# Kernel tuning notes

Measured on AMD Instinct MI355X. Metric: run time of the kernel, lower is better.

## Reference

```python
import jax, jax.numpy as jnp
import numpy as np

B, S, D = 4, 2048, 256
H = 8
HD = D // H
FF = 1024
LEN_M1 = 513


def _layer_norm(x, gamma, beta, eps=1e-5):
    m = jnp.mean(x, axis=-1, keepdims=True)
    v = jnp.var(x, axis=-1, keepdims=True)
    return (x - m) * jax.lax.rsqrt(v + eps) * gamma + beta


def setup_inputs() -> dict:
    key = jax.random.key(0)
    ks = jax.random.split(key, 16)
    s = 0.02  # init scale for weights
    return {
        "src": jax.random.normal(ks[0], (B, S, D), dtype=jnp.float32),
        "Wq": jax.random.normal(ks[1], (D, D), dtype=jnp.float32) * s,
        "bq": jnp.zeros((D,), dtype=jnp.float32),
        "Wk": jax.random.normal(ks[2], (D, D), dtype=jnp.float32) * s,
        "bk": jnp.zeros((D,), dtype=jnp.float32),
        "Wv": jax.random.normal(ks[3], (D, D), dtype=jnp.float32) * s,
        "bv": jnp.zeros((D,), dtype=jnp.float32),
        "Wo": jax.random.normal(ks[4], (D, D), dtype=jnp.float32) * s,
        "bo": jnp.zeros((D,), dtype=jnp.float32),
        "W1": jax.random.normal(ks[5], (FF, D), dtype=jnp.float32) * s,
        "b1": jnp.zeros((FF,), dtype=jnp.float32),
        "W2": jax.random.normal(ks[6], (D, FF), dtype=jnp.float32) * s,
        "b2": jnp.zeros((D,), dtype=jnp.float32),
        "g1": jnp.ones((D,), dtype=jnp.float32),
        "be1": jnp.zeros((D,), dtype=jnp.float32),
        "g2": jnp.ones((D,), dtype=jnp.float32),
        "be2": jnp.zeros((D,), dtype=jnp.float32),
        "len_m1": LEN_M1,
    }


def reference(src, Wq, bq, Wk, bk, Wv, bv, Wo, bo, W1, b1, W2, b2, g1, be1, g2, be2, len_m1):
    Bb, Ss, Dd = src.shape
    hd = Dd // H
    # projections (torch Linear: x @ W.T + b), split heads -> [B,H,S,hd]
    q = (src @ Wq.T + bq).reshape(Bb, Ss, H, hd).transpose(0, 2, 1, 3)
    k = (src @ Wk.T + bk).reshape(Bb, Ss, H, hd).transpose(0, 2, 1, 3)
    v = (src @ Wv.T + bv).reshape(Bb, Ss, H, hd).transpose(0, 2, 1, 3)
    scores = jnp.einsum("bhqd,bhkd->bhqk", q, k) / np.sqrt(hd).astype(np.float32)
    # causal mask + global prefix block: masked where j > i OR (i < len_m1 and j >= len_m1)
    i = jnp.arange(Ss)[:, None]
    j = jnp.arange(Ss)[None, :]
    mask = (j > i) | ((i < len_m1) & (j >= len_m1))
    scores = jnp.where(mask, -jnp.inf, scores)
    attn = jax.nn.softmax(scores, axis=-1)
    ao = jnp.einsum("bhqk,bhkd->bhqd", attn, v).transpose(0, 2, 1, 3).reshape(Bb, Ss, Dd)
    src2 = _layer_norm(src + (ao @ Wo.T + bo), g1, be1)
    ff = jax.nn.gelu(src2 @ W1.T + b1, approximate=False) @ W2.T + b2
    return _layer_norm(src2 + ff, g2, be2)
```

## Files before the change

### kernel.cpp

```cpp
#include <hip/hip_runtime.h>
#include <math.h>

#define NB 4
#define NS 2048
#define ND 256
#define NH 8
#define NHD 32
#define NFF 1024
#define NM (NB*NS)
#define KPAD 40
#define VSP 72
#define VTP 72
#define AS 264
#define QSCALE 0.2550181657f

typedef __attribute__((ext_vector_type(4))) short short4v;
typedef __attribute__((ext_vector_type(8))) short short8v;
typedef __attribute__((ext_vector_type(4))) float f32x4;
typedef unsigned short us;

__device__ __forceinline__ us f2bf(float f){
  union { float f; unsigned u; } c; c.f = f;
  unsigned u = c.u + 0x7fffu + ((c.u >> 16) & 1u);
  return (us)(u >> 16);
}

__device__ __forceinline__ float wsum(float v){
  #pragma unroll
  for(int o=32;o>0;o>>=1) v += __shfl_xor(v,o);
  return v;
}

__global__ __launch_bounds__(256) void prep_kernel(
    const float* __restrict__ src,
    const float* __restrict__ Wq, const float* __restrict__ Wk, const float* __restrict__ Wv,
    const float* __restrict__ Wo, const float* __restrict__ W1, const float* __restrict__ W2,
    const float* __restrict__ bq,
    us* __restrict__ X, us* __restrict__ Wqkvb, us* __restrict__ Wob,
    us* __restrict__ W1b, us* __restrict__ W2b, float* __restrict__ bqs){
  unsigned bid = blockIdx.x;
  if (bid == 1408){ bqs[threadIdx.x] = bq[threadIdx.x]*QSCALE; return; }
  unsigned u = bid*256u + threadIdx.x;
  const float* sp; us* dp; float sc = 1.f;
  if (u < 262144u){ sp = src + (size_t)u*8; dp = X + (size_t)u*8; }
  else {
    unsigned v = u - 262144u;
    if      (v <  8192u){ sp = Wq + (size_t)v*8;            dp = Wqkvb + (size_t)v*8;            sc = QSCALE; }
    else if (v < 16384u){ sp = Wk + (size_t)(v- 8192u)*8;   dp = Wqkvb + 65536 + (size_t)(v- 8192u)*8; }
    else if (v < 24576u){ sp = Wv + (size_t)(v-16384u)*8;   dp = Wqkvb + 131072 + (size_t)(v-16384u)*8; }
    else if (v < 32768u){ sp = Wo + (size_t)(v-24576u)*8;   dp = Wob + (size_t)(v-24576u)*8; }
    else if (v < 65536u){ sp = W1 + (size_t)(v-32768u)*8;   dp = W1b + (size_t)(v-32768u)*8; }
    else               { sp = W2 + (size_t)(v-65536u)*8;    dp = W2b + (size_t)(v-65536u)*8; }
  }
  float4 a = *(const float4*)sp, b = *(const float4*)(sp+4);
  short8v o;
  o[0]=(short)f2bf(a.x*sc); o[1]=(short)f2bf(a.y*sc); o[2]=(short)f2bf(a.z*sc); o[3]=(short)f2bf(a.w*sc);
  o[4]=(short)f2bf(b.x*sc); o[5]=(short)f2bf(b.y*sc); o[6]=(short)f2bf(b.z*sc); o[7]=(short)f2bf(b.w*sc);
  *(short8v*)dp = o;
}

template<int KTOT, int EPI>
__global__ __launch_bounds__(256) void gemm_kernel(
    const us* __restrict__ A, const us* __restrict__ W,
    const float* __restrict__ bias0, const float* __restrict__ bias1, const float* __restrict__ bias2,
    const float* __restrict__ resid,
    us* __restrict__ outb, us* __restrict__ outv, float* __restrict__ outf){
  __shared__ us Asl[64*AS];
  const int t = threadIdx.x, l = t&63, wv = t>>6;
  const int lx = l&15, lw = l>>4;
  const int m0 = blockIdx.y*64;
  const int n0 = blockIdx.x*128 + wv*32;

  f32x4 acc[4][2];
  #pragma unroll
  for(int mb=0;mb<4;mb++)
    #pragma unroll
    for(int nb=0;nb<2;nb++) acc[mb][nb] = (f32x4){0.f,0.f,0.f,0.f};

  for (int kc = 0; kc < KTOT; kc += 256){
    __syncthreads();
    #pragma unroll
    for (int it=0; it<8; it++){
      int idx = it*256 + t;
      int r = idx>>5, c = idx&31;
      *(short8v*)&Asl[r*AS + c*8] = *(const short8v*)(A + (size_t)(m0+r)*KTOT + kc + c*8);
    }
    __syncthreads();
    short8v bf[2][8];
    #pragma unroll
    for (int nb=0; nb<2; nb++)
      #pragma unroll
      for (int ks=0; ks<8; ks++)
        bf[nb][ks] = *(const short8v*)(W + (size_t)(n0 + nb*16 + lx)*KTOT + kc + ks*32 + 8*lw);
    #pragma unroll
    for (int ks=0; ks<8; ks++){
      short8v af[4];
      #pragma unroll
      for (int mb=0; mb<4; mb++)
        af[mb] = *(const short8v*)&Asl[(mb*16+lx)*AS + ks*32 + 8*lw];
      #pragma unroll
      for (int mb=0; mb<4; mb++){
        acc[mb][0] = __builtin_amdgcn_mfma_f32_16x16x32_bf16(af[mb], bf[0][ks], acc[mb][0], 0,0,0);
        acc[mb][1] = __builtin_amdgcn_mfma_f32_16x16x32_bf16(af[mb], bf[1][ks], acc[mb][1], 0,0,0);
      }
    }
  }
  const int mr0 = m0 + 4*lw;
  #pragma unroll
  for (int nb=0; nb<2; nb++){
    int n = n0 + nb*16 + lx;
    if (EPI == 0){
      int seg = n >> 8, nn = n & 255;
      const float* bp = (seg==0) ? bias0 : (seg==1) ? bias1 : bias2;
      float bb = bp[nn];
      if (seg < 2){
        us* op = outb + (size_t)seg*((size_t)NM*ND) + nn;
        #pragma unroll
        for (int mb=0; mb<4; mb++)
          #pragma unroll
          for (int r=0; r<4; r++)
            op[(size_t)(mr0 + mb*16 + r)*ND] = f2bf(acc[mb][nb][r] + bb);
      } else {
        int hh = nn >> 5, dd = nn & 31;
        int bidx = mr0 >> 11;
        int s0 = mr0 & 2047;
        us* vp = outv + (((size_t)bidx*NH + hh)*NHD + dd)*NS;
        #pragma unroll
        for (int mb=0; mb<4; mb++){
          short4v v4;
          #pragma unroll
          for (int r=0; r<4; r++) v4[r] = (short)f2bf(acc[mb][nb][r] + bb);
          *(short4v*)(vp + s0 + mb*16) = v4;
        }
      }
    } else if (EPI == 1 || EPI == 3){
      float bb = bias0[n];
      #pragma unroll
      for (int mb=0; mb<4; mb++)
        #pragma unroll
        for (int r=0; r<4; r++){
          size_t off = (size_t)(mr0 + mb*16 + r)*ND + n;
          outf[off] = acc[mb][nb][r] + bb + resid[off];
        }
    } else {
      float bb = bias0[n];
      #pragma unroll
      for (int mb=0; mb<4; mb++)
        #pragma unroll
        for (int r=0; r<4; r++){
          float x = acc[mb][nb][r] + bb;
          float g = 0.5f*x*(1.f + erff(x*0.70710678118654752f));
          outb[(size_t)(mr0 + mb*16 + r)*NFF + n] = f2bf(g);
        }
    }
  }
}

__global__ __launch_bounds__(256) void ln_kernel(
    const float* __restrict__ Xin, const float* __restrict__ g, const float* __restrict__ be,
    us* __restrict__ outb, float* __restrict__ outf){
  const int t = threadIdx.x, lane = t&63, wv = t>>6;
  const int m0 = blockIdx.x*16;
  #pragma unroll
  for(int rr=0; rr<4; rr++){
    int r = m0 + wv*4 + rr;
    const float* xr = Xin + (size_t)r*ND;
    float x[4]; float s=0.f,q=0.f;
    #pragma unroll
    for(int k=0;k<4;k++){ x[k]=xr[lane+64*k]; s+=x[k]; q+=x[k]*x[k]; }
    s = wsum(s); q = wsum(q);
    float mean = s*(1.f/ND), var = q*(1.f/ND)-mean*mean;
    float rstd = rsqrtf(var+1e-5f);
    #pragma unroll
    for(int k=0;k<4;k++){
      int col = lane+64*k;
      float y = (x[k]-mean)*rstd*g[col] + be[col];
      if (outf) outf[(size_t)r*ND+col] = y;
      if (outb) outb[(size_t)r*ND+col] = f2bf(y);
    }
  }
}

template<bool MASK>
__device__ __forceinline__ void attn_tile(
    const us* __restrict__ Kl, const us* __restrict__ Vl,
    const short8v qf, const int lx, const int lw, const int jt, const int qg,
    f32x4& acc0, f32x4& acc1, float& lsum){
  f32x4 s4[4];
  #pragma unroll
  for (int kb=0; kb<4; kb++){
    short8v kf = *(const short8v*)(Kl + (kb*16 + lx)*KPAD + 8*lw);
    f32x4 z = {0.f,0.f,0.f,0.f};
    s4[kb] = __builtin_amdgcn_mfma_f32_16x16x32_bf16(kf, qf, z, 0,0,0);
  }
  float p[16];
  #pragma unroll
  for (int kb=0; kb<4; kb++)
    #pragma unroll
    for (int r=0; r<4; r++){
      float x = exp2f(s4[kb][r]);
      if (MASK) x = ((jt + 16*kb + 4*lw + r) > qg) ? 0.f : x;
      p[kb*4+r] = x;
    }
  {
    float a0=p[0]+p[1],   a1=p[2]+p[3],   a2=p[4]+p[5],   a3=p[6]+p[7];
    float a4=p[8]+p[9],   a5=p[10]+p[11], a6=p[12]+p[13], a7=p[14]+p[15];
    float b0=a0+a1, b1=a2+a3, b2=a4+a5, b3=a6+a7;
    lsum += (b0+b1) + (b2+b3);
  }
  #pragma unroll
  for (int c=0; c<2; c++){
    unsigned w0,w1,w2,w3;
    asm("v_cvt_pk_bf16_f32 %0, %1, %2" : "=v"(w0) : "v"(p[8*c+0]), "v"(p[8*c+1]));
    asm("v_cvt_pk_bf16_f32 %0, %1, %2" : "=v"(w1) : "v"(p[8*c+2]), "v"(p[8*c+3]));
    asm("v_cvt_pk_bf16_f32 %0, %1, %2" : "=v"(w2) : "v"(p[8*c+4]), "v"(p[8*c+5]));
    asm("v_cvt_pk_bf16_f32 %0, %1, %2" : "=v"(w3) : "v"(p[8*c+6]), "v"(p[8*c+7]));
    union { unsigned u[4]; short8v v; } pu;
    pu.u[0]=w0; pu.u[1]=w1; pu.u[2]=w2; pu.u[3]=w3;
    short8v pf = pu.v;
    short8v aL = *(const short8v*)(Vl + (size_t)( lx    )*VSP + 32*c + 8*lw);
    short8v aH = *(const short8v*)(Vl + (size_t)(16+lx  )*VSP + 32*c + 8*lw);
    acc0 = __builtin_amdgcn_mfma_f32_16x16x32_bf16(aL, pf, acc0, 0,0,0);
    acc1 = __builtin_amdgcn_mfma_f32_16x16x32_bf16(aH, pf, acc1, 0,0,0);
  }
}

__global__ __launch_bounds__(256) void attn_kernel(
    const us* __restrict__ Q, const us* __restrict__ K,
    const us* __restrict__ Vt, us* __restrict__ AO){
  __shared__ us Klds[2][64*KPAD];
  __shared__ us Vs[2][32*VSP];
  __shared__ us Ex[4][16*VTP];

  const int t = threadIdx.x, l = t & 63, wv = t >> 6;
  const int lx = l & 15, lw = l >> 4;
  const int bid = blockIdx.x;
  const int qtile = 31 - (bid >> 5);
  const int bh = bid & 31;
  const int b = bh >> 3, h = bh & 7;
  const int qbase = qtile*64 + wv*16;
  const int qg = qbase + lx;

  const us* Qg = Q + ((size_t)b*NS)*ND + h*NHD;
  const us* Kg = K + ((size_t)b*NS)*ND + h*NHD;
  const us* Vg = Vt + (size_t)bh*NHD*NS;

  short8v qf = *(const short8v*)(Qg + (size_t)(qbase + lx)*ND + 8*lw);

  f32x4 acc0 = {0.f,0.f,0.f,0.f}, acc1 = {0.f,0.f,0.f,0.f};
  float lsum = 0.f;

  const int kr = t >> 2, kp = t & 3;
  const int vd = t >> 3, vp = t & 7;
  const int vS0 = 32*(vp>>2) + 16*(vp&1) + 4*((vp>>1)&1);
  const int jmax = qtile*64;

  {
    short8v k0 = *(const short8v*)(Kg + (size_t)kr*ND + kp*8);
    short8v v0 = *(const short8v*)(Vg + (size_t)vd*NS + vp*8);
    *(short8v*)&Klds[0][kr*KPAD + kp*8] = k0;
    short4v lo = {v0[0],v0[1],v0[2],v0[3]}, hi = {v0[4],v0[5],v0[6],v0[7]};
    *(short4v*)&Vs[0][vd*VSP + vS0]     = lo;
    *(short4v*)&Vs[0][vd*VSP + vS0 + 8] = hi;
  }
  __syncthreads();

  int cur = 0;
  for (int jt = 0; jt < jmax; jt += 64){
    short8v kn = *(const short8v*)(Kg + (size_t)(jt + 64 + kr)*ND + kp*8);
    short8v vn = *(const short8v*)(Vg + (size_t)vd*NS + (jt + 64) + vp*8);
    attn_tile<false>(&Klds[cur][0], &Vs[cur][0], qf, lx, lw, jt, qg, acc0, acc1, lsum);
    *(short8v*)&Klds[cur^1][kr*KPAD + kp*8] = kn;
    short4v lo = {vn[0],vn[1],vn[2],vn[3]}, hi = {vn[4],vn[5],vn[6],vn[7]};
    *(short4v*)&Vs[cur^1][vd*VSP + vS0]     = lo;
    *(short4v*)&Vs[cur^1][vd*VSP + vS0 + 8] = hi;
    __syncthreads();
    cur ^= 1;
  }
  attn_tile<true>(&Klds[cur][0], &Vs[cur][0], qf, lx, lw, jmax, qg, acc0, acc1, lsum);

  float lt = lsum + __shfl_xor(lsum, 16);
  lt += __shfl_xor(lt, 32);
  float inv = 1.f / lt;
  float* ol = (float*)&Ex[wv][0];
  #pragma unroll
  for (int r=0;r<4;r++){
    ol[lx*36 +      4*lw + r] = acc0[r]*inv;
    ol[lx*36 + 16 + 4*lw + r] = acc1[r]*inv;
  }
  int rr = l >> 2, cc = l & 3;
  const float* op8 = &ol[rr*36 + cc*8];
  short8v o8;
  #pragma unroll
  for (int j=0;j<8;j++) o8[j] = (short)f2bf(op8[j]);
  *(short8v*)(AO + ((size_t)(b*NS + qbase + rr))*ND + h*NHD + cc*8) = o8;
}

extern "C" void kernel_launch(void* const* d_in, const int* in_sizes, int n_in,
                              void* d_out, int out_size, void* d_ws, size_t ws_size,
                              hipStream_t stream){
  const float* src = (const float*)d_in[0];
  const float* Wq  = (const float*)d_in[1];
  const float* bq  = (const float*)d_in[2];
  const float* Wk  = (const float*)d_in[3];
  const float* bk  = (const float*)d_in[4];
  const float* Wv  = (const float*)d_in[5];
  const float* bv  = (const float*)d_in[6];
  const float* Wo  = (const float*)d_in[7];
  const float* bo  = (const float*)d_in[8];
  const float* W1  = (const float*)d_in[9];
  const float* b1  = (const float*)d_in[10];
  const float* W2  = (const float*)d_in[11];
  const float* b2  = (const float*)d_in[12];
  const float* g1  = (const float*)d_in[13];
  const float* be1 = (const float*)d_in[14];
  const float* g2  = (const float*)d_in[15];
  const float* be2 = (const float*)d_in[16];

  const size_t MB = 1048576;
  unsigned char* w8 = (unsigned char*)d_ws;
  us* X     = (us*)(w8 + 0);
  us* Qb    = (us*)(w8 + 4*MB);
  us* Kb    = (us*)(w8 + 8*MB);
  us* Vtg   = (us*)(w8 + 12*MB);
  us* AO    = (us*)(w8 + 16*MB);
  us* S2b   = (us*)(w8 + 20*MB);
  us* FF    = (us*)(w8 + 24*MB);
  us* Wqkvb = (us*)(w8 + 40*MB);
  us* Wob   = (us*)(w8 + 40*MB + 384*1024);
  us* W1b   = (us*)(w8 + 40*MB + 512*1024);
  us* W2b   = (us*)(w8 + 40*MB + 1024*1024);
  float* bqs   = (float*)(w8 + 40*MB + 1536*1024);
  float* S2pre = (float*)(w8 + 42*MB);
  float* S2f   = (float*)(w8 + 50*MB);
  float* Ypre  = (float*)(w8 + 0);
  float* out = (float*)d_out;

  prep_kernel<<<1409, 256, 0, stream>>>(src, Wq,Wk,Wv,Wo,W1,W2, bq,
                                        X, Wqkvb, Wob, W1b, W2b, bqs);
  gemm_kernel<256,0><<<dim3(6,128), 256, 0, stream>>>(X, Wqkvb, bqs, bk, bv, nullptr, Qb, Vtg, nullptr);
  attn_kernel<<<1024, 256, 0, stream>>>(Qb, Kb, Vtg, AO);
  gemm_kernel<256,1><<<dim3(2,128), 256, 0, stream>>>(AO, Wob, bo, nullptr, nullptr, src, nullptr, nullptr, S2pre);
  ln_kernel<<<NM/16, 256, 0, stream>>>(S2pre, g1, be1, S2b, S2f);
  gemm_kernel<256,2><<<dim3(8,128), 256, 0, stream>>>(S2b, W1b, b1, nullptr, nullptr, nullptr, FF, nullptr, nullptr);
  gemm_kernel<1024,3><<<dim3(2,128), 256, 0, stream>>>(FF, W2b, b2, nullptr, nullptr, S2f, nullptr, nullptr, Ypre);
  ln_kernel<<<NM/16, 256, 0, stream>>>(Ypre, g2, be2, nullptr, out);
}
```

Measured before the change: 106.5 us.

## Pair query tiles per attention block and read FFN residual as bf16

The attention kernel now runs 512-thread blocks that each handle two adjacent 64-row query tiles of one head. The K/V tiles are staged once for both tiles, with half the threads loading K and half loading V, and each wave applies the causal mask on its own diagonal tile. This halves redundant K/V global loads and LDS staging, and the new block ordering pairs early and late tiles to balance causal work. Separately, the final FFN GEMM reads the residual from the bf16 LayerNorm output instead of a separate fp32 copy, which drops one fp32 write and read but adds bf16 rounding error to the residual.

```diff
diff --git a/kernel.cpp b/kernel.cpp
--- a/kernel.cpp
+++ b/kernel.cpp
@@ -23,6 +23,9 @@
   union { float f; unsigned u; } c; c.f = f;
   unsigned u = c.u + 0x7fffu + ((c.u >> 16) & 1u);
   return (us)(u >> 16);
+}
+__device__ __forceinline__ float bf2f(us u){
+  union { unsigned u; float f; } c; c.u = ((unsigned)u) << 16; return c.f;
 }
 
 __device__ __forceinline__ float wsum(float v){
@@ -63,7 +66,7 @@
 __global__ __launch_bounds__(256) void gemm_kernel(
     const us* __restrict__ A, const us* __restrict__ W,
     const float* __restrict__ bias0, const float* __restrict__ bias1, const float* __restrict__ bias2,
-    const float* __restrict__ resid,
+    const float* __restrict__ resid, const us* __restrict__ residb,
     us* __restrict__ outb, us* __restrict__ outv, float* __restrict__ outf){
   __shared__ us Asl[64*AS];
   const int t = threadIdx.x, l = t&63, wv = t>>6;
@@ -133,7 +136,7 @@
           *(short4v*)(vp + s0 + mb*16) = v4;
         }
       }
-    } else if (EPI == 1 || EPI == 3){
+    } else if (EPI == 1){
       float bb = bias0[n];
       #pragma unroll
       for (int mb=0; mb<4; mb++)
@@ -141,6 +144,15 @@
         for (int r=0; r<4; r++){
           size_t off = (size_t)(mr0 + mb*16 + r)*ND + n;
           outf[off] = acc[mb][nb][r] + bb + resid[off];
+        }
+    } else if (EPI == 3){
+      float bb = bias0[n];
+      #pragma unroll
+      for (int mb=0; mb<4; mb++)
+        #pragma unroll
+        for (int r=0; r<4; r++){
+          size_t off = (size_t)(mr0 + mb*16 + r)*ND + n;
+          outf[off] = acc[mb][nb][r] + bb + bf2f(residb[off]);
         }
     } else {
       float bb = bias0[n];
@@ -225,21 +237,25 @@
   }
 }
 
-__global__ __launch_bounds__(256) void attn_kernel(
+__global__ __launch_bounds__(512) void attn_kernel(
     const us* __restrict__ Q, const us* __restrict__ K,
     const us* __restrict__ Vt, us* __restrict__ AO){
   __shared__ us Klds[2][64*KPAD];
   __shared__ us Vs[2][32*VSP];
-  __shared__ us Ex[4][16*VTP];
+  __shared__ us Ex[8][16*VTP];
 
   const int t = threadIdx.x, l = t & 63, wv = t >> 6;
   const int lx = l & 15, lw = l >> 4;
   const int bid = blockIdx.x;
-  const int qtile = 31 - (bid >> 5);
+  const int g = bid >> 5;
+  const int P = (g < 8) ? g : 23 - g;
   const int bh = bid & 31;
   const int b = bh >> 3, h = bh & 7;
-  const int qbase = qtile*64 + wv*16;
+  const int tile = 2*P + (wv >> 2);
+  const int qbase = tile*64 + (wv & 3)*16;
   const int qg = qbase + lx;
+  const int my_jmax = tile*64;
+  const int blk_jmax = (2*P + 1)*64;
 
   const us* Qg = Q + ((size_t)b*NS)*ND + h*NHD;
   const us* Kg = K + ((size_t)b*NS)*ND + h*NHD;
@@ -250,15 +266,16 @@
   f32x4 acc0 = {0.f,0.f,0.f,0.f}, acc1 = {0.f,0.f,0.f,0.f};
   float lsum = 0.f;
 
+  const bool isK = t < 256;
   const int kr = t >> 2, kp = t & 3;
-  const int vd = t >> 3, vp = t & 7;
+  const int tv = t - 256, vd = (tv >> 3) & 31, vp = tv & 7;
   const int vS0 = 32*(vp>>2) + 16*(vp&1) + 4*((vp>>1)&1);
-  const int jmax = qtile*64;
-
-  {
+
+  if (isK){
     short8v k0 = *(const short8v*)(Kg + (size_t)kr*ND + kp*8);
+    *(short8v*)&Klds[0][kr*KPAD + kp*8] = k0;
+  } else {
     short8v v0 = *(const short8v*)(Vg + (size_t)vd*NS + vp*8);
-    *(short8v*)&Klds[0][kr*KPAD + kp*8] = k0;
     short4v lo = {v0[0],v0[1],v0[2],v0[3]}, hi = {v0[4],v0[5],v0[6],v0[7]};
     *(short4v*)&Vs[0][vd*VSP + vS0]     = lo;
     *(short4v*)&Vs[0][vd*VSP + vS0 + 8] = hi;
@@ -266,18 +283,29 @@
   __syncthreads();
 
   int cur = 0;
-  for (int jt = 0; jt < jmax; jt += 64){
-    short8v kn = *(const short8v*)(Kg + (size_t)(jt + 64 + kr)*ND + kp*8);
-    short8v vn = *(const short8v*)(Vg + (size_t)vd*NS + (jt + 64) + vp*8);
-    attn_tile<false>(&Klds[cur][0], &Vs[cur][0], qf, lx, lw, jt, qg, acc0, acc1, lsum);
-    *(short8v*)&Klds[cur^1][kr*KPAD + kp*8] = kn;
-    short4v lo = {vn[0],vn[1],vn[2],vn[3]}, hi = {vn[4],vn[5],vn[6],vn[7]};
-    *(short4v*)&Vs[cur^1][vd*VSP + vS0]     = lo;
-    *(short4v*)&Vs[cur^1][vd*VSP + vS0 + 8] = hi;
+  for (int jt = 0; jt <= blk_jmax; jt += 64){
+    short8v nx;
+    const bool more = jt < blk_jmax;
+    if (more){
+      if (isK) nx = *(const short8v*)(Kg + (size_t)(jt + 64 + kr)*ND + kp*8);
+      else     nx = *(const short8v*)(Vg + (size_t)vd*NS + (jt + 64) + vp*8);
+    }
+    if (jt < my_jmax)
+      attn_tile<false>(&Klds[cur][0], &Vs[cur][0], qf, lx, lw, jt, qg, acc0, acc1, lsum);
+    else if (jt == my_jmax)
+      attn_tile<true>(&Klds[cur][0], &Vs[cur][0], qf, lx, lw, jt, qg, acc0, acc1, lsum);
+    if (more){
+      if (isK){
+        *(short8v*)&Klds[cur^1][kr*KPAD + kp*8] = nx;
+      } else {
+        short4v lo = {nx[0],nx[1],nx[2],nx[3]}, hi = {nx[4],nx[5],nx[6],nx[7]};
+        *(short4v*)&Vs[cur^1][vd*VSP + vS0]     = lo;
+        *(short4v*)&Vs[cur^1][vd*VSP + vS0 + 8] = hi;
+      }
+    }
     __syncthreads();
     cur ^= 1;
   }
-  attn_tile<true>(&Klds[cur][0], &Vs[cur][0], qf, lx, lw, jmax, qg, acc0, acc1, lsum);
 
   float lt = lsum + __shfl_xor(lsum, 16);
   lt += __shfl_xor(lt, 32);
@@ -332,17 +360,16 @@
   us* W2b   = (us*)(w8 + 40*MB + 1024*1024);
   float* bqs   = (float*)(w8 + 40*MB + 1536*1024);
   float* S2pre = (float*)(w8 + 42*MB);
-  float* S2f   = (float*)(w8 + 50*MB);
   float* Ypre  = (float*)(w8 + 0);
   float* out = (float*)d_out;
 
   prep_kernel<<<1409, 256, 0, stream>>>(src, Wq,Wk,Wv,Wo,W1,W2, bq,
                                         X, Wqkvb, Wob, W1b, W2b, bqs);
-  gemm_kernel<256,0><<<dim3(6,128), 256, 0, stream>>>(X, Wqkvb, bqs, bk, bv, nullptr, Qb, Vtg, nullptr);
-  attn_kernel<<<1024, 256, 0, stream>>>(Qb, Kb, Vtg, AO);
-  gemm_kernel<256,1><<<dim3(2,128), 256, 0, stream>>>(AO, Wob, bo, nullptr, nullptr, src, nullptr, nullptr, S2pre);
-  ln_kernel<<<NM/16, 256, 0, stream>>>(S2pre, g1, be1, S2b, S2f);
-  gemm_kernel<256,2><<<dim3(8,128), 256, 0, stream>>>(S2b, W1b, b1, nullptr, nullptr, nullptr, FF, nullptr, nullptr);
-  gemm_kernel<1024,3><<<dim3(2,128), 256, 0, stream>>>(FF, W2b, b2, nullptr, nullptr, S2f, nullptr, nullptr, Ypre);
+  gemm_kernel<256,0><<<dim3(6,128), 256, 0, stream>>>(X, Wqkvb, bqs, bk, bv, nullptr, nullptr, Qb, Vtg, nullptr);
+  attn_kernel<<<512, 512, 0, stream>>>(Qb, Kb, Vtg, AO);
+  gemm_kernel<256,1><<<dim3(2,128), 256, 0, stream>>>(AO, Wob, bo, nullptr, nullptr, src, nullptr, nullptr, nullptr, S2pre);
+  ln_kernel<<<NM/16, 256, 0, stream>>>(S2pre, g1, be1, S2b, nullptr);
+  gemm_kernel<256,2><<<dim3(8,128), 256, 0, stream>>>(S2b, W1b, b1, nullptr, nullptr, nullptr, nullptr, FF, nullptr, nullptr);
+  gemm_kernel<1024,3><<<dim3(2,128), 256, 0, stream>>>(FF, W2b, b2, nullptr, nullptr, nullptr, S2b, nullptr, nullptr, Ypre);
   ln_kernel<<<NM/16, 256, 0, stream>>>(Ypre, g2, be2, nullptr, out);
 }
```

Measured after the change: 112.4 us. 5.5% more time.
